# Optimization experiments

Hardware: AMD Instinct MI355X
Metric: run time of the kernel (lower is better)

The kernel has to match this reference:

```python
import jax, jax.numpy as jnp
import numpy as np

N, M = 4096, 8192
IN_DIM, OUT_DIM = 4096, 1024
NUM_SAMPLE = 10


def setup_inputs() -> dict:
    key = jax.random.key(0)
    k1, k2, k3, k4, k5 = jax.random.split(key, 5)
    node_features = jax.random.normal(k1, (N, IN_DIM), dtype=jnp.float32)
    neighbor_features = jax.random.normal(k2, (M, IN_DIM), dtype=jnp.float32)
    # Xavier-ish scale for params
    weight = jax.random.normal(k3, (OUT_DIM, IN_DIM), dtype=jnp.float32) * (1.0 / np.sqrt(IN_DIM))
    attention_vector = jax.random.normal(k4, (2 * OUT_DIM, 1), dtype=jnp.float32) * 0.05
    neighbor_idx = jax.random.randint(k5, (N, NUM_SAMPLE), 0, M, dtype=jnp.int32)
    return {
        "node_features": node_features,
        "neighbor_features": neighbor_features,
        "weight": weight,
        "attention_vector": attention_vector,
        "neighbor_idx": neighbor_idx,
    }


def reference(node_features, neighbor_features, weight, attention_vector, neighbor_idx):
    # Linear transform: [N, out], [M, out]
    node_t = node_features @ weight.T
    neigh_t = neighbor_features @ weight.T

    # combined @ attention_vector decomposes:
    # cat([h_i, h_j]) @ a == h_i @ a1 + h_j @ a2  (same math, no [N,M,2*out] tensor)
    a1 = attention_vector[:OUT_DIM, 0]   # [out]
    a2 = attention_vector[OUT_DIM:, 0]   # [out]
    scores = jax.nn.leaky_relu((node_t @ a1)[:, None] + (neigh_t @ a2)[None, :],
                               negative_slope=0.2)  # [N, M]

    # Build dense 0/1 mask from sampled neighbor indices (ragged -> dense)
    rows = jnp.arange(N, dtype=jnp.int32)[:, None]                  # [N,1]
    mask = jnp.zeros((N, M), dtype=jnp.float32).at[rows, neighbor_idx].set(1.0)

    scores = jnp.where(mask == 0, -jnp.inf, scores)
    attn = jax.nn.softmax(scores, axis=1)           # masked softmax over neighbor pool
    return attn @ neigh_t                           # [N, out]
```

## Files before the change

kernel.cpp:

```cpp
#include <hip/hip_runtime.h>

#define IN_DIM  4096
#define OUT_DIM 1024
#define NN      4096
#define MM      8192
#define NSAMP   10

typedef __bf16 bf16x8 __attribute__((ext_vector_type(8)));
typedef float  fx4    __attribute__((ext_vector_type(4)));

__device__ __forceinline__ ushort f2bf(float f) {
    union { float f; unsigned u; } v; v.f = f;
    unsigned u = v.u;
    return (ushort)((u + 0x7FFFu + ((u >> 16) & 1u)) >> 16);
}
__device__ __forceinline__ float bf2f(ushort u) {
    union { unsigned u; float f; } v; v.u = ((unsigned)u) << 16;
    return v.f;
}

#define GLDS(g, l) __builtin_amdgcn_global_load_lds(                           \
    (const __attribute__((address_space(1))) unsigned*)(g),                    \
    (__attribute__((address_space(3))) unsigned*)(l), 16, 0, 0)

__global__ __launch_bounds__(256) void k_attvec(const float* __restrict__ W,
                                                const float* __restrict__ att,
                                                float* __restrict__ v1,
                                                float* __restrict__ v2,
                                                ushort* __restrict__ Wbf) {
    int k  = blockIdx.x * 256 + threadIdx.x;
    int o0 = blockIdx.y * 16;
    float s1 = 0.f, s2 = 0.f;
#pragma unroll
    for (int o = o0; o < o0 + 16; ++o) {
        float w = W[(size_t)o * IN_DIM + k];
        Wbf[(size_t)o * IN_DIM + k] = f2bf(w);
        s1 += att[o] * w;
        s2 += att[OUT_DIM + o] * w;
    }
    atomicAdd(&v1[k], s1);
    atomicAdd(&v2[k], s2);
}

__global__ __launch_bounds__(256) void k_rows(const float* __restrict__ node_f,
                                              const float* __restrict__ neigh_f,
                                              const float* __restrict__ v1,
                                              const float* __restrict__ v2,
                                              float* __restrict__ nalpha,
                                              float* __restrict__ nbeta,
                                              ushort* __restrict__ Abf) {
    int row  = blockIdx.x * 4 + (threadIdx.x >> 6);
    int lane = threadIdx.x & 63;
    float s = 0.f;
    if (row < NN) {
        const float4* xr = reinterpret_cast<const float4*>(node_f + (size_t)row * IN_DIM);
        const float4* vr = reinterpret_cast<const float4*>(v1);
#pragma unroll
        for (int i = lane; i < IN_DIM / 4; i += 64) {
            float4 a = xr[i], b = vr[i];
            s += a.x * b.x + a.y * b.y + a.z * b.z + a.w * b.w;
        }
    } else {
        int j = row - NN;
        const float4* xr = reinterpret_cast<const float4*>(neigh_f + (size_t)j * IN_DIM);
        const float4* vr = reinterpret_cast<const float4*>(v2);
        ushort4* yr = reinterpret_cast<ushort4*>(Abf + (size_t)j * IN_DIM);
#pragma unroll
        for (int i = lane; i < IN_DIM / 4; i += 64) {
            float4 a = xr[i], b = vr[i];
            s += a.x * b.x + a.y * b.y + a.z * b.z + a.w * b.w;
            ushort4 o;
            o.x = f2bf(a.x); o.y = f2bf(a.y); o.z = f2bf(a.z); o.w = f2bf(a.w);
            yr[i] = o;
        }
    }
#pragma unroll
    for (int off = 32; off > 0; off >>= 1) s += __shfl_down(s, off, 64);
    if (lane == 0) {
        if (row < NN) nalpha[row] = s; else nbeta[row - NN] = s;
    }
}

#define TM 128
#define TN 128
#define BK 64
#define KSPLIT (IN_DIM / 2)

__global__ __launch_bounds__(256, 4) void k_gemm(const ushort* __restrict__ A,
                                                 const ushort* __restrict__ B,
                                                 ushort* __restrict__ P) {
    __shared__ __align__(16) ushort As[TM * BK];
    __shared__ __align__(16) ushort Bs[TN * BK];
    const int tid  = threadIdx.x;
    const int lane = tid & 63;
    const int wave = tid >> 6;
    const int wm   = (wave >> 1) * 64;
    const int wn   = (wave & 1) * 64;
    const int lrow = lane & 15;
    const int q    = lane >> 4;

    const int bm  = blockIdx.x * TM;
    const int bn  = blockIdx.y * TN;
    const int bz  = blockIdx.z;
    const int kb  = bz * KSPLIT;

    const int sr  = wave * 32 + (lane >> 3);
    const int sco = (((lane & 7) ^ (lane >> 3)) << 3);
    const ushort* gA = A + (size_t)(bm + sr) * IN_DIM + kb + sco;
    const ushort* gB = B + (size_t)(bn + sr) * IN_DIM + kb + sco;
    ushort* lA = As + wave * 2048;
    ushort* lB = Bs + wave * 2048;

    const int c0u = ((q ^ (lrow & 7)) << 3);

    fx4 acc[4][4] = {};

    for (int k0 = 0; k0 < KSPLIT; k0 += BK) {
#pragma unroll
        for (int i = 0; i < 4; ++i)
            GLDS(gA + k0 + (size_t)i * 8 * IN_DIM, lA + i * 512);
#pragma unroll
        for (int i = 0; i < 4; ++i)
            GLDS(gB + k0 + (size_t)i * 8 * IN_DIM, lB + i * 512);
        __syncthreads();

#pragma unroll
        for (int s = 0; s < 2; ++s) {
            const int co = c0u ^ (s << 5);
            bf16x8 af[4], bfr[4];
#pragma unroll
            for (int mi = 0; mi < 4; ++mi)
                af[mi] = *reinterpret_cast<const bf16x8*>(As + (wm + mi * 16 + lrow) * BK + co);
#pragma unroll
            for (int ni = 0; ni < 4; ++ni)
                bfr[ni] = *reinterpret_cast<const bf16x8*>(Bs + (wn + ni * 16 + lrow) * BK + co);
#pragma unroll
            for (int mi = 0; mi < 4; ++mi)
#pragma unroll
                for (int ni = 0; ni < 4; ++ni)
                    acc[mi][ni] = __builtin_amdgcn_mfma_f32_16x16x32_bf16(af[mi], bfr[ni], acc[mi][ni], 0, 0, 0);
        }
        __syncthreads();
    }

    ushort* Pz = P + (size_t)bz * MM * OUT_DIM;
#pragma unroll
    for (int mi = 0; mi < 4; ++mi)
#pragma unroll
        for (int ni = 0; ni < 4; ++ni) {
            int r = bm + wm + mi * 16 + q * 4;
            int c = bn + wn + ni * 16 + lrow;
#pragma unroll
            for (int v = 0; v < 4; ++v)
                Pz[(size_t)(r + v) * OUT_DIM + c] = f2bf(acc[mi][ni][v]);
        }
}

__global__ __launch_bounds__(256) void k_aggregate(const ushort* __restrict__ P,
                                                   const float* __restrict__ nalpha,
                                                   const float* __restrict__ nbeta,
                                                   const int* __restrict__ nidx,
                                                   float* __restrict__ outp) {
    int row = blockIdx.x;
    __shared__ int   s_idx[NSAMP];
    __shared__ float s_w[NSAMP];
    if (threadIdx.x < 16) {
        int t = threadIdx.x;
        int j = (t < NSAMP) ? nidx[row * NSAMP + t] : -1;
        float score = -INFINITY;
        if (t < NSAMP) {
            float x = nalpha[row] + nbeta[j];
            score = x > 0.f ? x : 0.2f * x;
        }
        bool dup = false;
#pragma unroll
        for (int sIdx = 0; sIdx < NSAMP; ++sIdx) {
            int js = __shfl(j, sIdx, 16);
            if (sIdx < t && js == j) dup = true;
        }
        float mx = score;
#pragma unroll
        for (int off = 8; off > 0; off >>= 1) {
            float o = __shfl_xor(mx, off, 16);
            mx = o > mx ? o : mx;
        }
        float e = (t < NSAMP && !dup) ? expf(score - mx) : 0.f;
        float sum = e;
#pragma unroll
        for (int off = 8; off > 0; off >>= 1) sum += __shfl_xor(sum, off, 16);
        if (t < NSAMP) {
            s_idx[t] = j;
            s_w[t]   = e / sum;
        }
    }
    __syncthreads();
    int col = threadIdx.x * 4;
    float ax = 0.f, ay = 0.f, az = 0.f, aw = 0.f;
#pragma unroll
    for (int t = 0; t < NSAMP; ++t) {
        float w = s_w[t];
        size_t off = (size_t)s_idx[t] * OUT_DIM + col;
        ushort4 u0 = *reinterpret_cast<const ushort4*>(P + off);
        ushort4 u1 = *reinterpret_cast<const ushort4*>(P + (size_t)MM * OUT_DIM + off);
        ax += w * (bf2f(u0.x) + bf2f(u1.x));
        ay += w * (bf2f(u0.y) + bf2f(u1.y));
        az += w * (bf2f(u0.z) + bf2f(u1.z));
        aw += w * (bf2f(u0.w) + bf2f(u1.w));
    }
    float4 o; o.x = ax; o.y = ay; o.z = az; o.w = aw;
    *reinterpret_cast<float4*>(outp + (size_t)row * OUT_DIM + col) = o;
}

extern "C" void kernel_launch(void* const* d_in, const int* in_sizes, int n_in,
                              void* d_out, int out_size, void* d_ws, size_t ws_size,
                              hipStream_t stream) {
    const float* node_f  = (const float*)d_in[0];
    const float* neigh_f = (const float*)d_in[1];
    const float* W       = (const float*)d_in[2];
    const float* att     = (const float*)d_in[3];
    const int*   nidx    = (const int*)d_in[4];
    float* outp = (float*)d_out;

    char* ws = (char*)d_ws;
    ushort* Abf = (ushort*)ws;
    ushort* Wbf = (ushort*)(ws + 67108864);
    ushort* P   = (ushort*)(ws + 75497472);
    float*  v1     = (float*)(ws + 109051904);
    float*  v2     = v1 + IN_DIM;
    float*  nalpha = v2 + IN_DIM;
    float*  nbeta  = nalpha + NN;

    hipMemsetAsync(v1, 0, 2 * IN_DIM * sizeof(float), stream);

    k_attvec   <<<dim3(16, 64),          256, 0, stream>>>(W, att, v1, v2, Wbf);
    k_rows     <<<(NN + MM) / 4,         256, 0, stream>>>(node_f, neigh_f, v1, v2, nalpha, nbeta, Abf);
    k_gemm     <<<dim3(64, 8, 2),        256, 0, stream>>>(Abf, Wbf, P);
    k_aggregate<<<NN,                    256, 0, stream>>>(P, nalpha, nbeta, nidx, outp);
}
```

Measured before the change: 369.4 us.

## Fuse neighbor bf16 conversion and beta dot product into GEMM A-tile loads

The GEMM now reads fp32 neighbor features directly, converts them to bf16 in registers and writes swizzled tiles into LDS. This removes the separate pass that wrote a 64MB bf16 copy of the neighbor matrix and read it back. The bn==0 blocks also compute the neighbor beta dot product with v2 staged in shared memory and accumulate it atomically. Node alpha moves to its own smaller kernel that keeps v1 in LDS. In exchange, the A-operand path loses the async global-to-LDS loads and each block's A reads double in fp32 size. The same A data is re-read and re-converted by all 8 column blocks, which adds VALU work and register pressure inside the GEMM loop.

```diff
diff --git a/kernel.cpp b/kernel.cpp
--- a/kernel.cpp
+++ b/kernel.cpp
@@ -8,6 +8,7 @@
 
 typedef __bf16 bf16x8 __attribute__((ext_vector_type(8)));
 typedef float  fx4    __attribute__((ext_vector_type(4)));
+typedef ushort u16x8  __attribute__((ext_vector_type(8)));
 
 __device__ __forceinline__ ushort f2bf(float f) {
     union { float f; unsigned u; } v; v.f = f;
@@ -42,43 +43,35 @@
     atomicAdd(&v2[k], s2);
 }
 
-__global__ __launch_bounds__(256) void k_rows(const float* __restrict__ node_f,
-                                              const float* __restrict__ neigh_f,
-                                              const float* __restrict__ v1,
-                                              const float* __restrict__ v2,
-                                              float* __restrict__ nalpha,
-                                              float* __restrict__ nbeta,
-                                              ushort* __restrict__ Abf) {
+__global__ __launch_bounds__(256) void k_rows_node(const float* __restrict__ node_f,
+                                                   const float* __restrict__ v1,
+                                                   float* __restrict__ nalpha) {
+    __shared__ __align__(16) float v1s[IN_DIM];
+#pragma unroll
+    for (int i = 0; i < 4; ++i)
+        *reinterpret_cast<float4*>(&v1s[threadIdx.x * 16 + i * 4]) =
+            *reinterpret_cast<const float4*>(&v1[threadIdx.x * 16 + i * 4]);
+    __syncthreads();
+
     int row  = blockIdx.x * 4 + (threadIdx.x >> 6);
     int lane = threadIdx.x & 63;
+    const float4* xr = reinterpret_cast<const float4*>(node_f + (size_t)row * IN_DIM);
+    const float4* vr = reinterpret_cast<const float4*>(v1s);
     float s = 0.f;
-    if (row < NN) {
-        const float4* xr = reinterpret_cast<const float4*>(node_f + (size_t)row * IN_DIM);
-        const float4* vr = reinterpret_cast<const float4*>(v1);
-#pragma unroll
-        for (int i = lane; i < IN_DIM / 4; i += 64) {
-            float4 a = xr[i], b = vr[i];
-            s += a.x * b.x + a.y * b.y + a.z * b.z + a.w * b.w;
-        }
-    } else {
-        int j = row - NN;
-        const float4* xr = reinterpret_cast<const float4*>(neigh_f + (size_t)j * IN_DIM);
-        const float4* vr = reinterpret_cast<const float4*>(v2);
-        ushort4* yr = reinterpret_cast<ushort4*>(Abf + (size_t)j * IN_DIM);
-#pragma unroll
-        for (int i = lane; i < IN_DIM / 4; i += 64) {
-            float4 a = xr[i], b = vr[i];
-            s += a.x * b.x + a.y * b.y + a.z * b.z + a.w * b.w;
-            ushort4 o;
-            o.x = f2bf(a.x); o.y = f2bf(a.y); o.z = f2bf(a.z); o.w = f2bf(a.w);
-            yr[i] = o;
+#pragma unroll
+    for (int half = 0; half < 2; ++half) {
+        float4 a[8];
+#pragma unroll
+        for (int i = 0; i < 8; ++i) a[i] = xr[lane + (half * 8 + i) * 64];
+#pragma unroll
+        for (int i = 0; i < 8; ++i) {
+            float4 b = vr[lane + (half * 8 + i) * 64];
+            s += a[i].x * b.x + a[i].y * b.y + a[i].z * b.z + a[i].w * b.w;
         }
     }
 #pragma unroll
     for (int off = 32; off > 0; off >>= 1) s += __shfl_down(s, off, 64);
-    if (lane == 0) {
-        if (row < NN) nalpha[row] = s; else nbeta[row - NN] = s;
-    }
+    if (lane == 0) nalpha[row] = s;
 }
 
 #define TM 128
@@ -86,11 +79,14 @@
 #define BK 64
 #define KSPLIT (IN_DIM / 2)
 
-__global__ __launch_bounds__(256, 4) void k_gemm(const ushort* __restrict__ A,
+__global__ __launch_bounds__(256, 4) void k_gemm(const float* __restrict__ Af,
                                                  const ushort* __restrict__ B,
-                                                 ushort* __restrict__ P) {
+                                                 ushort* __restrict__ P,
+                                                 const float* __restrict__ v2,
+                                                 float* __restrict__ nbeta) {
     __shared__ __align__(16) ushort As[TM * BK];
     __shared__ __align__(16) ushort Bs[TN * BK];
+    __shared__ __align__(16) float  v2s[KSPLIT];
     const int tid  = threadIdx.x;
     const int lane = tid & 63;
     const int wave = tid >> 6;
@@ -106,22 +102,53 @@
 
     const int sr  = wave * 32 + (lane >> 3);
     const int sco = (((lane & 7) ^ (lane >> 3)) << 3);
-    const ushort* gA = A + (size_t)(bm + sr) * IN_DIM + kb + sco;
     const ushort* gB = B + (size_t)(bn + sr) * IN_DIM + kb + sco;
-    ushort* lA = As + wave * 2048;
     ushort* lB = Bs + wave * 2048;
 
+    const int r = tid >> 1;
+    const int h = tid & 1;
+    const float* gA = Af + (size_t)(bm + r) * IN_DIM + kb + h * 32;
+    ushort* wA = As + r * 64;
+
+#pragma unroll
+    for (int i = 0; i < 2; ++i)
+        *reinterpret_cast<float4*>(&v2s[tid * 8 + i * 4]) =
+            *reinterpret_cast<const float4*>(&v2[kb + tid * 8 + i * 4]);
+    __syncthreads();
+
     const int c0u = ((q ^ (lrow & 7)) << 3);
+    const bool dofuse = (bn == 0);
+    float sdot = 0.f;
 
     fx4 acc[4][4] = {};
 
     for (int k0 = 0; k0 < KSPLIT; k0 += BK) {
-#pragma unroll
-        for (int i = 0; i < 4; ++i)
-            GLDS(gA + k0 + (size_t)i * 8 * IN_DIM, lA + i * 512);
 #pragma unroll
         for (int i = 0; i < 4; ++i)
             GLDS(gB + k0 + (size_t)i * 8 * IN_DIM, lB + i * 512);
+
+        float4 a8[8];
+#pragma unroll
+        for (int l = 0; l < 8; ++l)
+            a8[l] = *reinterpret_cast<const float4*>(gA + k0 + l * 4);
+
+        if (dofuse) {
+#pragma unroll
+            for (int l = 0; l < 8; ++l) {
+                float4 b = *reinterpret_cast<const float4*>(&v2s[k0 + h * 32 + l * 4]);
+                sdot += a8[l].x * b.x + a8[l].y * b.y + a8[l].z * b.z + a8[l].w * b.w;
+            }
+        }
+
+#pragma unroll
+        for (int cc = 0; cc < 4; ++cc) {
+            float4 u = a8[2 * cc], v = a8[2 * cc + 1];
+            u16x8 o;
+            o[0] = f2bf(u.x); o[1] = f2bf(u.y); o[2] = f2bf(u.z); o[3] = f2bf(u.w);
+            o[4] = f2bf(v.x); o[5] = f2bf(v.y); o[6] = f2bf(v.z); o[7] = f2bf(v.w);
+            const int p = ((h << 2) | cc) ^ (r & 7);
+            *reinterpret_cast<u16x8*>(wA + p * 8) = o;
+        }
         __syncthreads();
 
 #pragma unroll
@@ -143,16 +170,21 @@
         __syncthreads();
     }
 
+    if (dofuse) {
+        sdot += __shfl_xor(sdot, 1, 64);
+        if (h == 0) atomicAdd(&nbeta[bm + r], sdot);
+    }
+
     ushort* Pz = P + (size_t)bz * MM * OUT_DIM;
 #pragma unroll
     for (int mi = 0; mi < 4; ++mi)
 #pragma unroll
         for (int ni = 0; ni < 4; ++ni) {
-            int r = bm + wm + mi * 16 + q * 4;
-            int c = bn + wn + ni * 16 + lrow;
+            int rr = bm + wm + mi * 16 + q * 4;
+            int c  = bn + wn + ni * 16 + lrow;
 #pragma unroll
             for (int v = 0; v < 4; ++v)
-                Pz[(size_t)(r + v) * OUT_DIM + c] = f2bf(acc[mi][ni][v]);
+                Pz[(size_t)(rr + v) * OUT_DIM + c] = f2bf(acc[mi][ni][v]);
         }
 }
 
@@ -222,18 +254,17 @@
     float* outp = (float*)d_out;
 
     char* ws = (char*)d_ws;
-    ushort* Abf = (ushort*)ws;
-    ushort* Wbf = (ushort*)(ws + 67108864);
-    ushort* P   = (ushort*)(ws + 75497472);
-    float*  v1     = (float*)(ws + 109051904);
+    ushort* Wbf = (ushort*)ws;
+    ushort* P   = (ushort*)(ws + 8388608);
+    float*  v1     = (float*)(ws + 41943040);
     float*  v2     = v1 + IN_DIM;
-    float*  nalpha = v2 + IN_DIM;
-    float*  nbeta  = nalpha + NN;
-
-    hipMemsetAsync(v1, 0, 2 * IN_DIM * sizeof(float), stream);
-
-    k_attvec   <<<dim3(16, 64),          256, 0, stream>>>(W, att, v1, v2, Wbf);
-    k_rows     <<<(NN + MM) / 4,         256, 0, stream>>>(node_f, neigh_f, v1, v2, nalpha, nbeta, Abf);
-    k_gemm     <<<dim3(64, 8, 2),        256, 0, stream>>>(Abf, Wbf, P);
-    k_aggregate<<<NN,                    256, 0, stream>>>(P, nalpha, nbeta, nidx, outp);
-}
+    float*  nbeta  = v2 + IN_DIM;
+    float*  nalpha = nbeta + MM;
+
+    hipMemsetAsync(v1, 0, (2 * IN_DIM + MM) * sizeof(float), stream);
+
+    k_attvec   <<<dim3(16, 64),   256, 0, stream>>>(W, att, v1, v2, Wbf);
+    k_gemm     <<<dim3(64, 8, 2), 256, 0, stream>>>(neigh_f, Wbf, P, v2, nbeta);
+    k_rows_node<<<NN / 4,         256, 0, stream>>>(node_f, v1, nalpha);
+    k_aggregate<<<NN,             256, 0, stream>>>(P, nalpha, nbeta, nidx, outp);
+}
```

After: 412.1 us. +11.5%, slower.
